# Kernel tuning notes

Measured on AMD Instinct MI355X. Metric: run time of the kernel, lower is better.

The kernel has to match this reference:

```python
import jax, jax.numpy as jnp
import numpy as np

D_MODEL = 1024
NUM_HEADS = 16
D_K = D_MODEL // NUM_HEADS
ROPE_THETA = 10000.0


def setup_inputs() -> dict:
    key = jax.random.key(0)
    kx, kq, kk, kv, ko = jax.random.split(key, 5)
    B, S = 2, 2048
    sigma = np.sqrt(2.0) / np.sqrt(D_MODEL + D_MODEL)
    x = jax.random.normal(kx, (B, S, D_MODEL), dtype=jnp.float32)
    Wq = jax.random.normal(kq, (D_MODEL, D_MODEL), dtype=jnp.float32) * sigma
    Wk = jax.random.normal(kk, (D_MODEL, D_MODEL), dtype=jnp.float32) * sigma
    Wv = jax.random.normal(kv, (D_MODEL, D_MODEL), dtype=jnp.float32) * sigma
    Wo = jax.random.normal(ko, (D_MODEL, D_MODEL), dtype=jnp.float32) * sigma
    return {"x": x, "Wq": Wq, "Wk": Wk, "Wv": Wv, "Wo": Wo}


def _rope(t, positions):
    # t: [B, H, S, D_K], positions: [S]
    half = jnp.arange(0, D_K, 2, dtype=jnp.float32)          # [D_K/2]
    freqs = 1.0 / (ROPE_THETA ** (half / D_K))               # [D_K/2]
    angles = positions[:, None].astype(jnp.float32) * freqs  # [S, D_K/2]
    cos = jnp.cos(angles)
    sin = jnp.sin(angles)
    t_even = t[..., 0::2]
    t_odd = t[..., 1::2]
    even_rot = t_even * cos - t_odd * sin
    odd_rot = t_even * sin + t_odd * cos
    # interleave back to [..., D_K]
    return jnp.stack([even_rot, odd_rot], axis=-1).reshape(t.shape)


def reference(x, Wq, Wk, Wv, Wo):
    B, S, _ = x.shape
    # weight layout is [d_out, d_in]: y = x @ W.T
    def proj(W):
        y = jnp.einsum('bsd,ed->bse', x, W)
        return y.reshape(B, S, NUM_HEADS, D_K).transpose(0, 2, 1, 3)  # [B,H,S,Dk]
    Q, K, V = proj(Wq), proj(Wk), proj(Wv)
    positions = jnp.arange(S)
    Q = _rope(Q, positions)
    K = _rope(K, positions)
    scale = 1.0 / jnp.sqrt(jnp.asarray(D_K, dtype=x.dtype))
    scores = jnp.einsum('bhqd,bhkd->bhqk', Q, K) * scale  # [B,H,S,S]
    causal = jnp.tril(jnp.ones((S, S), dtype=bool))
    scores = jnp.where(causal, scores, -jnp.inf)
    probs = jax.nn.softmax(scores, axis=-1)
    out = jnp.einsum('bhqk,bhkd->bhqd', probs, V)          # [B,H,S,Dk]
    out = out.transpose(0, 2, 1, 3).reshape(B, S, D_MODEL)
    return jnp.einsum('bsd,ed->bse', out, Wo)
```

## Files before the change

### kernel.cpp

```cpp
#include <hip/hip_runtime.h>
#include <hip/hip_bf16.h>
#include <math.h>

#define S_LEN   2048
#define BATCH   2
#define DMODEL  1024
#define NHEADS  16
#define DKH     64
#define MROWS   (BATCH * S_LEN)

#define SPLIT_Q0   17
#define NPIECE     47
#define SLOTS_BH   30
#define PO_FLOATS  (960 * 4096)

typedef __attribute__((ext_vector_type(8)))  __bf16 bf16x8;
typedef __attribute__((ext_vector_type(4)))  float  f32x4;
typedef __attribute__((ext_vector_type(16))) float  f32x16;
typedef __attribute__((ext_vector_type(8)))  unsigned short u16x8;

__device__ __forceinline__ float bfu2f(unsigned short u) {
    union { unsigned int i; float f; } v;
    v.i = ((unsigned int)u) << 16;
    return v.f;
}

__device__ __forceinline__ unsigned short f2bfu(float f) {
    union { __bf16 h; unsigned short u; } v;
    v.h = (__bf16)f;
    return v.u;
}

#define LGKM0() __builtin_amdgcn_s_waitcnt(0xc07f)

#define VMCNT_BAR(n) do {                                        \
    asm volatile("s_waitcnt vmcnt(" #n ")" ::: "memory");        \
    __builtin_amdgcn_s_barrier();                                \
    __builtin_amdgcn_sched_barrier(0);                           \
} while (0)

__device__ __forceinline__ void gload_lds16(const void* g, void* l) {
    __builtin_amdgcn_global_load_lds(
        (const __attribute__((address_space(1))) void*)g,
        (__attribute__((address_space(3))) void*)l, 16, 0, 0);
}

__global__ __launch_bounds__(256) void cvt_all(
    const float* __restrict__ W0, const float* __restrict__ W1, const float* __restrict__ W2,
    const float* __restrict__ X,
    unsigned short* __restrict__ Wb, unsigned short* __restrict__ Xb)
{
    const int y = blockIdx.y;
    const float* src;
    unsigned short* dst;
    if (y < 3) {
        src = (y == 0) ? W0 : (y == 1) ? W1 : W2;
        dst = Wb + (size_t)y * (DMODEL * DMODEL);
    } else {
        src = X + (size_t)(y - 3) * (DMODEL * DMODEL);
        dst = Xb + (size_t)(y - 3) * (DMODEL * DMODEL);
    }
    size_t idx = ((size_t)blockIdx.x * 256 + threadIdx.x) * 8;
    float4 a = *(const float4*)(src + idx);
    float4 b = *(const float4*)(src + idx + 4);
    u16x8 h;
    h[0] = f2bfu(a.x); h[1] = f2bfu(a.y); h[2] = f2bfu(a.z); h[3] = f2bfu(a.w);
    h[4] = f2bfu(b.x); h[5] = f2bfu(b.y); h[6] = f2bfu(b.z); h[7] = f2bfu(b.w);
    *(u16x8*)(dst + idx) = h;
}

__global__ __launch_bounds__(256) void cvt_wo(
    const float* __restrict__ W, unsigned short* __restrict__ Wob)
{
    size_t idx = ((size_t)blockIdx.x * 256 + threadIdx.x) * 8;
    float4 a = *(const float4*)(W + idx);
    float4 b = *(const float4*)(W + idx + 4);
    u16x8 h;
    h[0] = f2bfu(a.x); h[1] = f2bfu(a.y); h[2] = f2bfu(a.z); h[3] = f2bfu(a.w);
    h[4] = f2bfu(b.x); h[5] = f2bfu(b.y); h[6] = f2bfu(b.z); h[7] = f2bfu(b.w);
    *(u16x8*)(Wob + idx) = h;
}

__global__ __launch_bounds__(256) void gemm_qkv(
    const unsigned short* __restrict__ Xb,
    const unsigned short* __restrict__ Wb,
    unsigned short* __restrict__ Yq, unsigned short* __restrict__ Yk, unsigned short* __restrict__ Yv)
{
    __shared__ __align__(16) unsigned char pool[49152];
    unsigned short* base = (unsigned short*)pool;

    const int tid  = threadIdx.x;
    const int wave = tid >> 6;
    const int lane = tid & 63;
    const int c    = lane & 15;
    const int quad = lane >> 4;

    const int m0 = blockIdx.y * 128;
    const int n0 = blockIdx.x * 128;
    const int w_idx = n0 >> 10;
    const int e0    = n0 & 1023;
    const unsigned short* Wsrc = Wb + (size_t)w_idx * (DMODEL * DMODEL);

    const int mhalf = (wave & 1) * 64;
    const int nhalf = (wave >> 1) * 64;

    f32x4 acc[4][4];
#pragma unroll
    for (int i = 0; i < 4; i++)
#pragma unroll
        for (int j = 0; j < 4; j++) acc[i][j] = (f32x4){0.f, 0.f, 0.f, 0.f};

    const int srow = wave * 32 + (lane >> 2);
    const int scol = (lane & 3) * 8;
    const unsigned short* Asrc = Xb   + (size_t)(m0 + srow) * DMODEL + scol;
    const unsigned short* Bsrc = Wsrc + (size_t)(e0 + srow) * DMODEL + scol;
    const int doff = srow * 32 + scol;

#define QKV_STAGE(buf, kt) do {                                                    \
    unsigned short* _A = base + (buf) * 8192;                                      \
    unsigned short* _B = _A + 4096;                                                \
    const int _k0 = (kt) * 32;                                                     \
    _Pragma("unroll")                                                              \
    for (int _j = 0; _j < 2; _j++) {                                               \
        gload_lds16(Asrc + (size_t)(_j * 16) * DMODEL + _k0, _A + doff + _j * 512);\
        gload_lds16(Bsrc + (size_t)(_j * 16) * DMODEL + _k0, _B + doff + _j * 512);\
    }                                                                              \
} while (0)

#define QKV_COMPUTE(buf) do {                                                      \
    const unsigned short* _A = base + (buf) * 8192;                                \
    const unsigned short* _B = _A + 4096;                                          \
    bf16x8 af[4], bfr[4];                                                          \
    _Pragma("unroll")                                                              \
    for (int mt = 0; mt < 4; mt++)                                                 \
        af[mt] = *(const bf16x8*)(&_A[(mhalf + mt * 16 + c) * 32 + quad * 8]);     \
    _Pragma("unroll")                                                              \
    for (int nt = 0; nt < 4; nt++)                                                 \
        bfr[nt] = *(const bf16x8*)(&_B[(nhalf + nt * 16 + c) * 32 + quad * 8]);    \
    _Pragma("unroll")                                                              \
    for (int mt = 0; mt < 4; mt++)                                                 \
        _Pragma("unroll")                                                          \
        for (int nt = 0; nt < 4; nt++)                                             \
            acc[mt][nt] = __builtin_amdgcn_mfma_f32_16x16x32_bf16(af[mt], bfr[nt], acc[mt][nt], 0, 0, 0); \
} while (0)

    QKV_STAGE(0, 0);
    QKV_STAGE(1, 1);
    for (int g = 0; g < 10; ++g) {
        const int t = g * 3;
        VMCNT_BAR(4); QKV_STAGE(2, t + 2); QKV_COMPUTE(0);
        VMCNT_BAR(4); QKV_STAGE(0, t + 3); QKV_COMPUTE(1);
        VMCNT_BAR(4); QKV_STAGE(1, t + 4); QKV_COMPUTE(2);
    }
    VMCNT_BAR(4); QKV_COMPUTE(0);
    VMCNT_BAR(0); QKV_COMPUTE(1);

    __syncthreads();

    const int h = (e0 + nhalf) >> 6;
    if (w_idx < 2) {
        unsigned short* Yqk = (w_idx == 0) ? Yq : Yk;
        float* EPf = (float*)pool + wave * 16 * 68;
        const int row = lane >> 2;
        const int cg  = lane & 3;
#pragma unroll
        for (int mt = 0; mt < 4; mt++) {
            LGKM0();
#pragma unroll
            for (int nt = 0; nt < 4; nt++)
#pragma unroll
                for (int r = 0; r < 4; r++)
                    EPf[(quad * 4 + r) * 68 + nt * 16 + c] = acc[mt][nt][r];
            LGKM0();
            float fl[16];
#pragma unroll
            for (int j = 0; j < 4; j++) {
                float4 v = *(const float4*)(&EPf[row * 68 + cg * 16 + j * 4]);
                fl[j * 4 + 0] = v.x; fl[j * 4 + 1] = v.y;
                fl[j * 4 + 2] = v.z; fl[j * 4 + 3] = v.w;
            }
            int m = m0 + mhalf + mt * 16 + row;
            int s = m & (S_LEN - 1);
            int b = m >> 11;
            u16x8 o0, o1;
#pragma unroll
            for (int pi = 0; pi < 8; pi++) {
                int p = cg * 8 + pi;
                float freq  = exp2f(-(float)p * 0.41524101186092034f);
                float angle = (float)s * freq;
                float sn, cs;
                __sincosf(angle, &sn, &cs);
                float ev = fl[2 * pi], ov = fl[2 * pi + 1];
                float re = ev * cs - ov * sn;
                float ro = ev * sn + ov * cs;
                if (pi < 4) { o0[2 * pi] = f2bfu(re); o0[2 * pi + 1] = f2bfu(ro); }
                else        { o1[2 * (pi - 4)] = f2bfu(re); o1[2 * (pi - 4) + 1] = f2bfu(ro); }
            }
            unsigned short* dst = Yqk + (((size_t)(b * NHEADS + h)) * S_LEN + s) * DKH + cg * 16;
            *(u16x8*)(dst)     = o0;
            *(u16x8*)(dst + 8) = o1;
        }
    } else {
        unsigned short* EPb = (unsigned short*)pool + wave * 64 * 72;
        LGKM0();
#pragma unroll
        for (int nt = 0; nt < 4; nt++)
#pragma unroll
            for (int mt = 0; mt < 4; mt++)
#pragma unroll
                for (int r = 0; r < 4; r++)
                    EPb[(nt * 16 + c) * 72 + mt * 16 + quad * 4 + r] = f2bfu(acc[mt][nt][r]);
        LGKM0();
        int mbase = m0 + mhalf;
        int s0 = mbase & (S_LEN - 1);
        int b  = mbase >> 11;
        unsigned short* dst = Yv + (((size_t)(b * NHEADS + h)) * DKH + lane) * S_LEN + s0;
#pragma unroll
        for (int j = 0; j < 8; j++)
            *(u16x8*)(dst + j * 8) = *(const u16x8*)(&EPb[lane * 72 + j * 8]);
    }
#undef QKV_STAGE
#undef QKV_COMPUTE
}

__global__ __launch_bounds__(256) void gemm_wo(
    const unsigned short* __restrict__ X,
    const unsigned short* __restrict__ Wob,
    float* __restrict__ Yf)
{
    __shared__ __align__(16) unsigned char pool[36864];
    unsigned short* base = (unsigned short*)pool;

    const int tid  = threadIdx.x;
    const int wave = tid >> 6;
    const int lane = tid & 63;
    const int c    = lane & 15;
    const int quad = lane >> 4;

    const int m0 = blockIdx.y * 64;
    const int n0 = blockIdx.x * 128;

    const int mhalf = (wave & 1) * 32;
    const int nhalf = (wave >> 1) * 64;

    f32x4 acc[2][4];
#pragma unroll
    for (int i = 0; i < 2; i++)
#pragma unroll
        for (int j = 0; j < 4; j++) acc[i][j] = (f32x4){0.f, 0.f, 0.f, 0.f};

    const int arow = wave * 16 + (lane >> 2);
    const int brow = wave * 32 + (lane >> 2);
    const int scol = (lane & 3) * 8;
    const unsigned short* Asrc = X   + (size_t)(m0 + arow) * DMODEL + scol;
    const unsigned short* Bsrc = Wob + (size_t)(n0 + brow) * DMODEL + scol;
    const int adoff = arow * 32 + scol;
    const int bdoff = brow * 32 + scol;

#define WO_STAGE(buf, kt) do {                                                     \
    unsigned short* _A = base + (buf) * 6144;                                      \
    unsigned short* _B = _A + 2048;                                                \
    const int _k0 = (kt) * 32;                                                     \
    gload_lds16(Asrc + _k0, _A + adoff);                                           \
    _Pragma("unroll")                                                              \
    for (int _j = 0; _j < 2; _j++)                                                 \
        gload_lds16(Bsrc + (size_t)(_j * 16) * DMODEL + _k0, _B + bdoff + _j * 512);\
} while (0)

#define WO_COMPUTE(buf) do {                                                       \
    const unsigned short* _A = base + (buf) * 6144;                                \
    const unsigned short* _B = _A + 2048;                                          \
    bf16x8 af[2], bfr[4];                                                          \
    _Pragma("unroll")                                                              \
    for (int mt = 0; mt < 2; mt++)                                                 \
        af[mt] = *(const bf16x8*)(&_A[(mhalf + mt * 16 + c) * 32 + quad * 8]);     \
    _Pragma("unroll")                                                              \
    for (int nt = 0; nt < 4; nt++)                                                 \
        bfr[nt] = *(const bf16x8*)(&_B[(nhalf + nt * 16 + c) * 32 + quad * 8]);    \
    _Pragma("unroll")                                                              \
    for (int mt = 0; mt < 2; mt++)                                                 \
        _Pragma("unroll")                                                          \
        for (int nt = 0; nt < 4; nt++)                                             \
            acc[mt][nt] = __builtin_amdgcn_mfma_f32_16x16x32_bf16(af[mt], bfr[nt], acc[mt][nt], 0, 0, 0); \
} while (0)

    WO_STAGE(0, 0);
    WO_STAGE(1, 1);
    for (int g = 0; g < 10; ++g) {
        const int t = g * 3;
        VMCNT_BAR(3); WO_STAGE(2, t + 2); WO_COMPUTE(0);
        VMCNT_BAR(3); WO_STAGE(0, t + 3); WO_COMPUTE(1);
        VMCNT_BAR(3); WO_STAGE(1, t + 4); WO_COMPUTE(2);
    }
    VMCNT_BAR(3); WO_COMPUTE(0);
    VMCNT_BAR(0); WO_COMPUTE(1);

    __syncthreads();

    float* EPf = (float*)pool + wave * 16 * 68;
    const int row = lane >> 2;
    const int cg  = lane & 3;
#pragma unroll
    for (int mt = 0; mt < 2; mt++) {
        LGKM0();
#pragma unroll
        for (int nt = 0; nt < 4; nt++)
#pragma unroll
            for (int r = 0; r < 4; r++)
                EPf[(quad * 4 + r) * 68 + nt * 16 + c] = acc[mt][nt][r];
        LGKM0();
        int m = m0 + mhalf + mt * 16 + row;
        float* dst = Yf + (size_t)m * DMODEL + n0 + nhalf + cg * 16;
#pragma unroll
        for (int j = 0; j < 4; j++)
            *(float4*)(dst + j * 4) = *(const float4*)(&EPf[row * 68 + cg * 16 + j * 4]);
    }
#undef WO_STAGE
#undef WO_COMPUTE
}

__global__ __launch_bounds__(128, 4) void attn_mfma(
    const unsigned short* __restrict__ Q,
    const unsigned short* __restrict__ K,
    const unsigned short* __restrict__ Vt,
    unsigned short* __restrict__ A,
    float* __restrict__ Scr)
{
    __shared__ unsigned short Ks[2][32 * 72];
    __shared__ unsigned short Vs[2][64 * 40];

    const int tid  = threadIdx.x;
    const int wave = tid >> 6;
    const int lane = tid & 63;
    const int c32  = lane & 31;
    const int hi   = lane >> 5;

    const int bh = blockIdx.x;
    const int b  = bh >> 4;
    const int h  = bh & 15;

    const int R = (int)blockIdx.y;
    int qb, t_lo, t_hi, spl = 0;
    bool is_split;
    if (R <= 16) {
        qb = 16 - R; t_lo = 0; t_hi = 2 * qb + 2; is_split = false;
    } else {
        int i = R - 17;
        qb  = 31 - (i >> 1);
        spl = i & 1;
        int nk = 2 * qb + 2, half = nk >> 1;
        t_lo = spl ? half : 0;
        t_hi = spl ? nk   : half;
        is_split = true;
    }
    const int q0b = qb * 64;
    const int q0w = q0b + wave * 32;

    const unsigned short* Qb = Q  + (size_t)bh * S_LEN * DKH;
    const unsigned short* Kb = K  + (size_t)bh * S_LEN * DKH;
    const unsigned short* Vb = Vt + (size_t)bh * DKH * S_LEN;

    bf16x8 qf0 = *(const bf16x8*)(Qb + (size_t)(q0w + c32) * DKH +  0 + hi * 8);
    bf16x8 qf1 = *(const bf16x8*)(Qb + (size_t)(q0w + c32) * DKH + 16 + hi * 8);
    bf16x8 qf2 = *(const bf16x8*)(Qb + (size_t)(q0w + c32) * DKH + 32 + hi * 8);
    bf16x8 qf3 = *(const bf16x8*)(Qb + (size_t)(q0w + c32) * DKH + 48 + hi * 8);

    f32x16 oA, oB;
#pragma unroll
    for (int r = 0; r < 16; r++) { oA[r] = 0.f; oB[r] = 0.f; }
    float lacc = 0.f;

    const int my_nkb = (q0w >> 5) + 1;
    const int kbf    = q0w >> 5;

    const int krow = tid >> 2;
    const int kcol = (tid & 3) * 16;
    const int vrow = tid >> 1;
    const int vcol = (tid & 1) * 16;

    uint4 gK0 = *(const uint4*)(Kb + (size_t)(t_lo * 32 + krow) * DKH + kcol);
    uint4 gK1 = *(const uint4*)(Kb + (size_t)(t_lo * 32 + krow) * DKH + kcol + 8);
    uint4 gV0 = *(const uint4*)(Vb + (size_t)vrow * S_LEN + t_lo * 32 + vcol);
    uint4 gV1 = *(const uint4*)(Vb + (size_t)vrow * S_LEN + t_lo * 32 + vcol + 8);
    *(uint4*)(&Ks[t_lo & 1][krow * 72 + kcol])     = gK0;
    *(uint4*)(&Ks[t_lo & 1][krow * 72 + kcol + 8]) = gK1;
    *(uint4*)(&Vs[t_lo & 1][vrow * 40 + vcol])     = gV0;
    *(uint4*)(&Vs[t_lo & 1][vrow * 40 + vcol + 8]) = gV1;

    for (int kb = t_lo; kb < t_hi; kb++) {
        const int k0 = kb * 32;
        const int nb = kb + 1;
        const bool pre = nb < t_hi;
        __syncthreads();
        if (pre) {
            gK0 = *(const uint4*)(Kb + (size_t)(nb * 32 + krow) * DKH + kcol);
            gK1 = *(const uint4*)(Kb + (size_t)(nb * 32 + krow) * DKH + kcol + 8);
            gV0 = *(const uint4*)(Vb + (size_t)vrow * S_LEN + nb * 32 + vcol);
            gV1 = *(const uint4*)(Vb + (size_t)vrow * S_LEN + nb * 32 + vcol + 8);
        }
        if (kb < my_nkb) {
            const unsigned short* Kc = &Ks[kb & 1][0];
            const unsigned short* Vc = &Vs[kb & 1][0];
            bf16x8 kf0 = *(const bf16x8*)(&Kc[c32 * 72 +  0 + hi * 8]);
            bf16x8 kf1 = *(const bf16x8*)(&Kc[c32 * 72 + 16 + hi * 8]);
            bf16x8 kf2 = *(const bf16x8*)(&Kc[c32 * 72 + 32 + hi * 8]);
            bf16x8 kf3 = *(const bf16x8*)(&Kc[c32 * 72 + 48 + hi * 8]);
            f32x16 s;
#pragma unroll
            for (int r = 0; r < 16; r++) s[r] = 0.f;
            __builtin_amdgcn_s_setprio(1);
            s = __builtin_amdgcn_mfma_f32_32x32x16_bf16(kf0, qf0, s, 0, 0, 0);
            s = __builtin_amdgcn_mfma_f32_32x32x16_bf16(kf1, qf1, s, 0, 0, 0);
            s = __builtin_amdgcn_mfma_f32_32x32x16_bf16(kf2, qf2, s, 0, 0, 0);
            s = __builtin_amdgcn_mfma_f32_32x32x16_bf16(kf3, qf3, s, 0, 0, 0);
            __builtin_amdgcn_s_setprio(0);
            float p[16];
            if (kb < kbf) {
#pragma unroll
                for (int r = 0; r < 16; r++) p[r] = __expf(s[r] * 0.125f);
            } else {
                const int qg = q0w + c32;
#pragma unroll
                for (int r = 0; r < 16; r++) {
                    int kg = k0 + (r & 3) + 8 * (r >> 2) + 4 * hi;
                    p[r] = (kg <= qg) ? __expf(s[r] * 0.125f) : 0.0f;
                }
            }
            unsigned pk[8];
#pragma unroll
            for (int i = 0; i < 8; i++) {
                asm("v_cvt_pk_bf16_f32 %0, %1, %2"
                    : "=v"(pk[i]) : "v"(p[2 * i]), "v"(p[2 * i + 1]));
                union { unsigned u; float f; } lo, hx;
                lo.u = pk[i] << 16;
                hx.u = pk[i] & 0xffff0000u;
                lacc += lo.f + hx.f;
            }
            unsigned f0[4], f1[4];
            {
                unsigned ta, tb;
                ta = (unsigned)__shfl_xor((int)pk[2], 32, 64);
                tb = (unsigned)__shfl_xor((int)pk[0], 32, 64);
                f0[0] = hi ? ta : pk[0];  f0[2] = hi ? pk[2] : tb;
                ta = (unsigned)__shfl_xor((int)pk[3], 32, 64);
                tb = (unsigned)__shfl_xor((int)pk[1], 32, 64);
                f0[1] = hi ? ta : pk[1];  f0[3] = hi ? pk[3] : tb;
                ta = (unsigned)__shfl_xor((int)pk[6], 32, 64);
                tb = (unsigned)__shfl_xor((int)pk[4], 32, 64);
                f1[0] = hi ? ta : pk[4];  f1[2] = hi ? pk[6] : tb;
                ta = (unsigned)__shfl_xor((int)pk[7], 32, 64);
                tb = (unsigned)__shfl_xor((int)pk[5], 32, 64);
                f1[1] = hi ? ta : pk[5];  f1[3] = hi ? pk[7] : tb;
            }
            union { unsigned u[4]; bf16x8 v; } pa0, pa1;
            pa0.u[0] = f0[0]; pa0.u[1] = f0[1]; pa0.u[2] = f0[2]; pa0.u[3] = f0[3];
            pa1.u[0] = f1[0]; pa1.u[1] = f1[1]; pa1.u[2] = f1[2]; pa1.u[3] = f1[3];
            bf16x8 v00 = *(const bf16x8*)(&Vc[(c32)      * 40 +  0 + hi * 8]);
            bf16x8 v10 = *(const bf16x8*)(&Vc[(c32)      * 40 + 16 + hi * 8]);
            bf16x8 v01 = *(const bf16x8*)(&Vc[(32 + c32) * 40 +  0 + hi * 8]);
            bf16x8 v11 = *(const bf16x8*)(&Vc[(32 + c32) * 40 + 16 + hi * 8]);
            __builtin_amdgcn_s_setprio(1);
            oA = __builtin_amdgcn_mfma_f32_32x32x16_bf16(pa0.v, v00, oA, 0, 0, 0);
            oA = __builtin_amdgcn_mfma_f32_32x32x16_bf16(pa1.v, v10, oA, 0, 0, 0);
            oB = __builtin_amdgcn_mfma_f32_32x32x16_bf16(pa0.v, v01, oB, 0, 0, 0);
            oB = __builtin_amdgcn_mfma_f32_32x32x16_bf16(pa1.v, v11, oB, 0, 0, 0);
            __builtin_amdgcn_s_setprio(0);
        }
        if (pre) {
            *(uint4*)(&Ks[nb & 1][krow * 72 + kcol])     = gK0;
            *(uint4*)(&Ks[nb & 1][krow * 72 + kcol + 8]) = gK1;
            *(uint4*)(&Vs[nb & 1][vrow * 40 + vcol])     = gV0;
            *(uint4*)(&Vs[nb & 1][vrow * 40 + vcol + 8]) = gV1;
        }
    }

    lacc += __shfl_xor(lacc, 32, 64);

    if (!is_split) {
        float inv = 1.0f / lacc;
#pragma unroll
        for (int r = 0; r < 16; r++) {
            int qr = (r & 3) + 8 * (r >> 2) + 4 * hi;
            float invr = __shfl(inv, qr, 64);
            int sg = q0w + qr;
            unsigned short* Ap = A + ((size_t)b * S_LEN + sg) * DMODEL + h * DKH;
            Ap[c32]      = f2bfu(oA[r] * invr);
            Ap[32 + c32] = f2bfu(oB[r] * invr);
        }
    } else {
        const int slot = bh * SLOTS_BH + (qb - SPLIT_Q0) * 2 + spl;
        float* Po = Scr + (size_t)slot * 4096;
        float* Pl = Scr + PO_FLOATS + (size_t)slot * 64;
#pragma unroll
        for (int r = 0; r < 16; r++) {
            int qr  = (r & 3) + 8 * (r >> 2) + 4 * hi;
            int row = wave * 32 + qr;
            Po[row * 64 + c32]      = oA[r];
            Po[row * 64 + 32 + c32] = oB[r];
        }
        if (hi == 0) Pl[wave * 32 + c32] = lacc;
    }
}

__global__ __launch_bounds__(256) void attn_combine(
    const float* __restrict__ Scr, unsigned short* __restrict__ A)
{
    const int bx  = blockIdx.x;
    const int bh  = bx / 15;
    const int qbm = bx % 15;
    const int qb  = SPLIT_Q0 + qbm;
    const int b   = bh >> 4;
    const int h   = bh & 15;

    const int slot0 = bh * SLOTS_BH + qbm * 2;
    const float* O0 = Scr + (size_t)slot0 * 4096;
    const float* O1 = O0 + 4096;
    const float* L0 = Scr + PO_FLOATS + (size_t)slot0 * 64;
    const float* L1 = L0 + 64;

    const int r  = threadIdx.x >> 2;
    const int cg = (threadIdx.x & 3) * 16;

    float inv = 1.0f / (L0[r] + L1[r]);

    u16x8 outv[2];
#pragma unroll
    for (int half = 0; half < 2; half++) {
        float4 a0 = *(const float4*)(O0 + r * 64 + cg + half * 8);
        float4 b0 = *(const float4*)(O0 + r * 64 + cg + half * 8 + 4);
        float4 a1 = *(const float4*)(O1 + r * 64 + cg + half * 8);
        float4 b1 = *(const float4*)(O1 + r * 64 + cg + half * 8 + 4);
        outv[half][0] = f2bfu((a0.x + a1.x) * inv);
        outv[half][1] = f2bfu((a0.y + a1.y) * inv);
        outv[half][2] = f2bfu((a0.z + a1.z) * inv);
        outv[half][3] = f2bfu((a0.w + a1.w) * inv);
        outv[half][4] = f2bfu((b0.x + b1.x) * inv);
        outv[half][5] = f2bfu((b0.y + b1.y) * inv);
        outv[half][6] = f2bfu((b0.z + b1.z) * inv);
        outv[half][7] = f2bfu((b0.w + b1.w) * inv);
    }
    const int s = qb * 64 + r;
    unsigned short* Ap = A + ((size_t)b * S_LEN + s) * DMODEL + h * DKH + cg;
    *(u16x8*)(Ap)     = outv[0];
    *(u16x8*)(Ap + 8) = outv[1];
}

extern "C" void kernel_launch(void* const* d_in, const int* in_sizes, int n_in,
                              void* d_out, int out_size, void* d_ws, size_t ws_size,
                              hipStream_t stream) {
    const float* x  = (const float*)d_in[0];
    const float* Wq = (const float*)d_in[1];
    const float* Wk = (const float*)d_in[2];
    const float* Wv = (const float*)d_in[3];
    const float* Wo = (const float*)d_in[4];
    float* out = (float*)d_out;

    unsigned short* Qw = (unsigned short*)d_ws;
    unsigned short* Kw = Qw + (size_t)MROWS * DMODEL;
    unsigned short* Vw = Kw + (size_t)MROWS * DMODEL;
    unsigned short* Wb = Vw + (size_t)MROWS * DMODEL;
    unsigned short* Aw = Wb;
    unsigned short* Wob = Qw;
    unsigned short* Xb = (unsigned short*)d_out;
    float* Scr = (float*)d_out;

    cvt_all<<<dim3(DMODEL * DMODEL / (256 * 8), 7), 256, 0, stream>>>(Wq, Wk, Wv, x, Wb, Xb);

    gemm_qkv<<<dim3(3 * DMODEL / 128, MROWS / 128), 256, 0, stream>>>(
        Xb, Wb, Qw, Kw, Vw);

    attn_mfma<<<dim3(NHEADS * BATCH, NPIECE), 128, 0, stream>>>(Qw, Kw, Vw, Aw, Scr);

    attn_combine<<<dim3(NHEADS * BATCH * 15), 256, 0, stream>>>(Scr, Aw);

    cvt_wo<<<dim3(DMODEL * DMODEL / (256 * 8)), 256, 0, stream>>>(Wo, Wob);

    gemm_wo<<<dim3(DMODEL / 128, MROWS / 64), 256, 0, stream>>>(Aw, Wob, out);
}
```

Before: 182.2 us.

## Split attention KV range across waves with per-wave LDS buffers and in-block combine

Each block now handles a 32-row query tile. Its two waves split the key-block range, and each wave has private double-buffered K/V tiles in LDS, so the per-iteration __syncthreads is gone. The partial outputs and row sums from the two waves are merged through shared memory, and long tiles are still split across two blocks that are combined by a second kernel. The aim is finer work granularity and no block-wide barriers in the inner loop, at the cost of more LDS per block (lower occupancy hint), more blocks, and extra combine traffic.

```diff
diff --git a/kernel.cpp b/kernel.cpp
--- a/kernel.cpp
+++ b/kernel.cpp
@@ -9,10 +9,9 @@
 #define DKH     64
 #define MROWS   (BATCH * S_LEN)
 
-#define SPLIT_Q0   17
-#define NPIECE     47
-#define SLOTS_BH   30
-#define PO_FLOATS  (960 * 4096)
+#define QT_SPLIT   34
+#define NPIECE_Y   94
+#define PO2_FLOATS (1920 * 2048)
 
 typedef __attribute__((ext_vector_type(8)))  __bf16 bf16x8;
 typedef __attribute__((ext_vector_type(4)))  float  f32x4;
@@ -319,15 +318,14 @@
 #undef WO_COMPUTE
 }
 
-__global__ __launch_bounds__(128, 4) void attn_mfma(
+__global__ __launch_bounds__(128, 2) void attn_mfma(
     const unsigned short* __restrict__ Q,
     const unsigned short* __restrict__ K,
     const unsigned short* __restrict__ Vt,
     unsigned short* __restrict__ A,
     float* __restrict__ Scr)
 {
-    __shared__ unsigned short Ks[2][32 * 72];
-    __shared__ unsigned short Vs[2][64 * 40];
+    __shared__ __align__(16) unsigned char pool[38912];
 
     const int tid  = threadIdx.x;
     const int wave = tid >> 6;
@@ -340,67 +338,79 @@
     const int h  = bh & 15;
 
     const int R = (int)blockIdx.y;
-    int qb, t_lo, t_hi, spl = 0;
+    int qt, c_lo, c_hi, spl = 0;
     bool is_split;
-    if (R <= 16) {
-        qb = 16 - R; t_lo = 0; t_hi = 2 * qb + 2; is_split = false;
+    if (R < 60) {
+        qt  = 63 - (R >> 1);
+        spl = R & 1;
+        int n = qt + 1;
+        c_lo = spl ? QT_SPLIT : 0;
+        c_hi = spl ? n : QT_SPLIT;
+        is_split = true;
     } else {
-        int i = R - 17;
-        qb  = 31 - (i >> 1);
-        spl = i & 1;
-        int nk = 2 * qb + 2, half = nk >> 1;
-        t_lo = spl ? half : 0;
-        t_hi = spl ? nk   : half;
-        is_split = true;
-    }
-    const int q0b = qb * 64;
-    const int q0w = q0b + wave * 32;
+        qt = 93 - R;
+        c_lo = 0; c_hi = qt + 1;
+        is_split = false;
+    }
+    const int q0t  = qt * 32;
+    const int mlen = c_hi - c_lo;
+    const int hf   = (mlen + 1) >> 1;
+    const int w_lo = c_lo + (wave ? hf : 0);
+    const int w_hi = wave ? c_hi : (c_lo + hf);
 
     const unsigned short* Qb = Q  + (size_t)bh * S_LEN * DKH;
     const unsigned short* Kb = K  + (size_t)bh * S_LEN * DKH;
     const unsigned short* Vb = Vt + (size_t)bh * DKH * S_LEN;
 
-    bf16x8 qf0 = *(const bf16x8*)(Qb + (size_t)(q0w + c32) * DKH +  0 + hi * 8);
-    bf16x8 qf1 = *(const bf16x8*)(Qb + (size_t)(q0w + c32) * DKH + 16 + hi * 8);
-    bf16x8 qf2 = *(const bf16x8*)(Qb + (size_t)(q0w + c32) * DKH + 32 + hi * 8);
-    bf16x8 qf3 = *(const bf16x8*)(Qb + (size_t)(q0w + c32) * DKH + 48 + hi * 8);
+    bf16x8 qf0 = *(const bf16x8*)(Qb + (size_t)(q0t + c32) * DKH +  0 + hi * 8);
+    bf16x8 qf1 = *(const bf16x8*)(Qb + (size_t)(q0t + c32) * DKH + 16 + hi * 8);
+    bf16x8 qf2 = *(const bf16x8*)(Qb + (size_t)(q0t + c32) * DKH + 32 + hi * 8);
+    bf16x8 qf3 = *(const bf16x8*)(Qb + (size_t)(q0t + c32) * DKH + 48 + hi * 8);
 
     f32x16 oA, oB;
 #pragma unroll
     for (int r = 0; r < 16; r++) { oA[r] = 0.f; oB[r] = 0.f; }
     float lacc = 0.f;
 
-    const int my_nkb = (q0w >> 5) + 1;
-    const int kbf    = q0w >> 5;
-
-    const int krow = tid >> 2;
-    const int kcol = (tid & 3) * 16;
-    const int vrow = tid >> 1;
-    const int vcol = (tid & 1) * 16;
-
-    uint4 gK0 = *(const uint4*)(Kb + (size_t)(t_lo * 32 + krow) * DKH + kcol);
-    uint4 gK1 = *(const uint4*)(Kb + (size_t)(t_lo * 32 + krow) * DKH + kcol + 8);
-    uint4 gV0 = *(const uint4*)(Vb + (size_t)vrow * S_LEN + t_lo * 32 + vcol);
-    uint4 gV1 = *(const uint4*)(Vb + (size_t)vrow * S_LEN + t_lo * 32 + vcol + 8);
-    *(uint4*)(&Ks[t_lo & 1][krow * 72 + kcol])     = gK0;
-    *(uint4*)(&Ks[t_lo & 1][krow * 72 + kcol + 8]) = gK1;
-    *(uint4*)(&Vs[t_lo & 1][vrow * 40 + vcol])     = gV0;
-    *(uint4*)(&Vs[t_lo & 1][vrow * 40 + vcol + 8]) = gV1;
-
-    for (int kb = t_lo; kb < t_hi; kb++) {
-        const int k0 = kb * 32;
-        const int nb = kb + 1;
-        const bool pre = nb < t_hi;
-        __syncthreads();
-        if (pre) {
-            gK0 = *(const uint4*)(Kb + (size_t)(nb * 32 + krow) * DKH + kcol);
-            gK1 = *(const uint4*)(Kb + (size_t)(nb * 32 + krow) * DKH + kcol + 8);
-            gV0 = *(const uint4*)(Vb + (size_t)vrow * S_LEN + nb * 32 + vcol);
-            gV1 = *(const uint4*)(Vb + (size_t)vrow * S_LEN + nb * 32 + vcol + 8);
-        }
-        if (kb < my_nkb) {
-            const unsigned short* Kc = &Ks[kb & 1][0];
-            const unsigned short* Vc = &Vs[kb & 1][0];
+    unsigned short* Ksw = (unsigned short*)(pool + wave * 9216);
+    unsigned short* Vsw = (unsigned short*)(pool + 18432 + wave * 10240);
+
+    const int krow = lane >> 1;
+    const int kcol = (lane & 1) * 32;
+
+    uint4 gK0, gK1, gK2, gK3, gV0, gV1, gV2, gV3;
+
+#define ATT_LOAD(t) do {                                                           \
+    const unsigned short* _kp = Kb + (size_t)((t) * 32 + krow) * DKH + kcol;       \
+    gK0 = *(const uint4*)(_kp);      gK1 = *(const uint4*)(_kp + 8);               \
+    gK2 = *(const uint4*)(_kp + 16); gK3 = *(const uint4*)(_kp + 24);              \
+    const unsigned short* _vp = Vb + (size_t)lane * S_LEN + (t) * 32;              \
+    gV0 = *(const uint4*)(_vp);      gV1 = *(const uint4*)(_vp + 8);               \
+    gV2 = *(const uint4*)(_vp + 16); gV3 = *(const uint4*)(_vp + 24);              \
+} while (0)
+
+#define ATT_WRITE(buf) do {                                                        \
+    unsigned short* _kd = Ksw + (buf) * 2304 + krow * 72 + kcol;                   \
+    *(uint4*)(_kd) = gK0;      *(uint4*)(_kd + 8) = gK1;                           \
+    *(uint4*)(_kd + 16) = gK2; *(uint4*)(_kd + 24) = gK3;                          \
+    unsigned short* _vd = Vsw + (buf) * 2560 + lane * 40;                          \
+    *(uint4*)(_vd) = gV0;      *(uint4*)(_vd + 8) = gV1;                           \
+    *(uint4*)(_vd + 16) = gV2; *(uint4*)(_vd + 24) = gV3;                          \
+} while (0)
+
+    if (w_lo < w_hi) {
+        ATT_LOAD(w_lo);
+        ATT_WRITE(0);
+        for (int kb = w_lo; kb < w_hi; kb++) {
+            const int cur = (kb - w_lo) & 1;
+            const int k0  = kb * 32;
+            const bool pre = (kb + 1) < w_hi;
+            if (pre) ATT_LOAD(kb + 1);
+            LGKM0();
+            __builtin_amdgcn_sched_barrier(0);
+
+            const unsigned short* Kc = Ksw + cur * 2304;
+            const unsigned short* Vc = Vsw + cur * 2560;
             bf16x8 kf0 = *(const bf16x8*)(&Kc[c32 * 72 +  0 + hi * 8]);
             bf16x8 kf1 = *(const bf16x8*)(&Kc[c32 * 72 + 16 + hi * 8]);
             bf16x8 kf2 = *(const bf16x8*)(&Kc[c32 * 72 + 32 + hi * 8]);
@@ -415,11 +425,11 @@
             s = __builtin_amdgcn_mfma_f32_32x32x16_bf16(kf3, qf3, s, 0, 0, 0);
             __builtin_amdgcn_s_setprio(0);
             float p[16];
-            if (kb < kbf) {
+            if (kb < qt) {
 #pragma unroll
                 for (int r = 0; r < 16; r++) p[r] = __expf(s[r] * 0.125f);
             } else {
-                const int qg = q0w + c32;
+                const int qg = q0t + c32;
 #pragma unroll
                 for (int r = 0; r < 16; r++) {
                     int kg = k0 + (r & 3) + 8 * (r >> 2) + 4 * hi;
@@ -465,58 +475,73 @@
             oB = __builtin_amdgcn_mfma_f32_32x32x16_bf16(pa0.v, v01, oB, 0, 0, 0);
             oB = __builtin_amdgcn_mfma_f32_32x32x16_bf16(pa1.v, v11, oB, 0, 0, 0);
             __builtin_amdgcn_s_setprio(0);
+
+            if (pre) ATT_WRITE(cur ^ 1);
         }
-        if (pre) {
-            *(uint4*)(&Ks[nb & 1][krow * 72 + kcol])     = gK0;
-            *(uint4*)(&Ks[nb & 1][krow * 72 + kcol + 8]) = gK1;
-            *(uint4*)(&Vs[nb & 1][vrow * 40 + vcol])     = gV0;
-            *(uint4*)(&Vs[nb & 1][vrow * 40 + vcol + 8]) = gV1;
-        }
-    }
+    }
+#undef ATT_LOAD
+#undef ATT_WRITE
 
     lacc += __shfl_xor(lacc, 32, 64);
 
+    __syncthreads();
+    float* comb = (float*)pool;
+    float* lc   = (float*)pool + 2 * 2048;
+#pragma unroll
+    for (int r = 0; r < 16; r++) {
+        int qr = (r & 3) + 8 * (r >> 2) + 4 * hi;
+        comb[wave * 2048 + qr * 64 + c32]      = oA[r];
+        comb[wave * 2048 + qr * 64 + 32 + c32] = oB[r];
+    }
+    if (hi == 0) lc[wave * 32 + c32] = lacc;
+    __syncthreads();
+
+    const int row = wave * 16 + (lane >> 2);
+    const int cg  = (lane & 3) * 16;
+    float lsum = lc[row] + lc[32 + row];
+    float vals[16];
+#pragma unroll
+    for (int j = 0; j < 4; j++) {
+        float4 a0 = *(const float4*)(&comb[row * 64 + cg + j * 4]);
+        float4 a1 = *(const float4*)(&comb[2048 + row * 64 + cg + j * 4]);
+        vals[j * 4 + 0] = a0.x + a1.x; vals[j * 4 + 1] = a0.y + a1.y;
+        vals[j * 4 + 2] = a0.z + a1.z; vals[j * 4 + 3] = a0.w + a1.w;
+    }
     if (!is_split) {
-        float inv = 1.0f / lacc;
-#pragma unroll
-        for (int r = 0; r < 16; r++) {
-            int qr = (r & 3) + 8 * (r >> 2) + 4 * hi;
-            float invr = __shfl(inv, qr, 64);
-            int sg = q0w + qr;
-            unsigned short* Ap = A + ((size_t)b * S_LEN + sg) * DMODEL + h * DKH;
-            Ap[c32]      = f2bfu(oA[r] * invr);
-            Ap[32 + c32] = f2bfu(oB[r] * invr);
-        }
+        float inv = 1.0f / lsum;
+        u16x8 o0, o1;
+#pragma unroll
+        for (int j = 0; j < 8; j++) { o0[j] = f2bfu(vals[j] * inv); o1[j] = f2bfu(vals[8 + j] * inv); }
+        int s = q0t + row;
+        unsigned short* Ap = A + ((size_t)b * S_LEN + s) * DMODEL + h * DKH + cg;
+        *(u16x8*)(Ap)     = o0;
+        *(u16x8*)(Ap + 8) = o1;
     } else {
-        const int slot = bh * SLOTS_BH + (qb - SPLIT_Q0) * 2 + spl;
-        float* Po = Scr + (size_t)slot * 4096;
-        float* Pl = Scr + PO_FLOATS + (size_t)slot * 64;
-#pragma unroll
-        for (int r = 0; r < 16; r++) {
-            int qr  = (r & 3) + 8 * (r >> 2) + 4 * hi;
-            int row = wave * 32 + qr;
-            Po[row * 64 + c32]      = oA[r];
-            Po[row * 64 + 32 + c32] = oB[r];
-        }
-        if (hi == 0) Pl[wave * 32 + c32] = lacc;
-    }
-}
-
-__global__ __launch_bounds__(256) void attn_combine(
+        const int slot = (bh * 30 + (qt - QT_SPLIT)) * 2 + spl;
+        float* Po = Scr + (size_t)slot * 2048;
+#pragma unroll
+        for (int j = 0; j < 4; j++)
+            *(float4*)(&Po[row * 64 + cg + j * 4]) =
+                (float4){vals[j * 4 + 0], vals[j * 4 + 1], vals[j * 4 + 2], vals[j * 4 + 3]};
+        if ((lane & 3) == 0) Scr[PO2_FLOATS + (size_t)slot * 32 + row] = lsum;
+    }
+}
+
+__global__ __launch_bounds__(128) void attn_combine(
     const float* __restrict__ Scr, unsigned short* __restrict__ A)
 {
     const int bx  = blockIdx.x;
-    const int bh  = bx / 15;
-    const int qbm = bx % 15;
-    const int qb  = SPLIT_Q0 + qbm;
+    const int bh  = bx / 30;
+    const int qtm = bx % 30;
+    const int qt  = QT_SPLIT + qtm;
     const int b   = bh >> 4;
     const int h   = bh & 15;
 
-    const int slot0 = bh * SLOTS_BH + qbm * 2;
-    const float* O0 = Scr + (size_t)slot0 * 4096;
-    const float* O1 = O0 + 4096;
-    const float* L0 = Scr + PO_FLOATS + (size_t)slot0 * 64;
-    const float* L1 = L0 + 64;
+    const int slot0 = (bh * 30 + qtm) * 2;
+    const float* O0 = Scr + (size_t)slot0 * 2048;
+    const float* O1 = O0 + 2048;
+    const float* L0 = Scr + PO2_FLOATS + (size_t)slot0 * 32;
+    const float* L1 = L0 + 32;
 
     const int r  = threadIdx.x >> 2;
     const int cg = (threadIdx.x & 3) * 16;
@@ -539,7 +564,7 @@
         outv[half][6] = f2bfu((b0.z + b1.z) * inv);
         outv[half][7] = f2bfu((b0.w + b1.w) * inv);
     }
-    const int s = qb * 64 + r;
+    const int s = qt * 32 + r;
     unsigned short* Ap = A + ((size_t)b * S_LEN + s) * DMODEL + h * DKH + cg;
     *(u16x8*)(Ap)     = outv[0];
     *(u16x8*)(Ap + 8) = outv[1];
@@ -569,9 +594,9 @@
     gemm_qkv<<<dim3(3 * DMODEL / 128, MROWS / 128), 256, 0, stream>>>(
         Xb, Wb, Qw, Kw, Vw);
 
-    attn_mfma<<<dim3(NHEADS * BATCH, NPIECE), 128, 0, stream>>>(Qw, Kw, Vw, Aw, Scr);
-
-    attn_combine<<<dim3(NHEADS * BATCH * 15), 256, 0, stream>>>(Scr, Aw);
+    attn_mfma<<<dim3(NHEADS * BATCH, NPIECE_Y), 128, 0, stream>>>(Qw, Kw, Vw, Aw, Scr);
+
+    attn_combine<<<dim3(NHEADS * BATCH * 30), 128, 0, stream>>>(Scr, Aw);
 
     cvt_wo<<<dim3(DMODEL * DMODEL / (256 * 8)), 256, 0, stream>>>(Wo, Wob);
 
```

Measured after the change: 201.5 us. 1.11x slower.
